# Kernel optimization log

Hardware: AMD Instinct MI355X
Metric: run time of the kernel (lower is better)

The kernel has to match this reference:

```python
import jax, jax.numpy as jnp
import numpy as np

IN_C, OUT_C, K = 32, 3, 4
FT_DIM = IN_C // 2            # 16
LIN_IN = 4 + FT_DIM           # 20
D = IN_C * OUT_C * K * K      # 1536
D8, D4, D2 = D // 8, D // 4, D // 2


def _geometry(h_in, w_in, h_out, w_out, k):
    # numpy replica of get_offset_scale (all-static shapes)
    ih = np.arange(1, h_out + 1, dtype=np.float32)
    iw = np.arange(1, w_out + 1, dtype=np.float32)
    sh, sw = float(h_out) / h_in, float(w_out) / w_in
    ch = ih / sh + 0.5 * (1 - 1 / sh) - 1.0
    cw = iw / sw + 0.5 * (1 - 1 / sw) - 1.0
    s = -((k - 1) // 2)
    gh = np.floor(np.floor(ch)[:, None] + np.arange(s, k + s, dtype=np.float32)).reshape(-1)
    gw = np.floor(np.floor(cw)[:, None] + np.arange(s, k + s, dtype=np.float32)).reshape(-1)
    IH, IW = np.meshgrid(gh, gw, indexing='ij')                 # [h*k, w*k]
    indice = np.stack([IH, IW], -1).reshape(h_out, k, w_out, k, 2).transpose(0, 2, 1, 3, 4)  # [h,w,k,k,2]
    CH, CW = np.meshgrid(ch, cw, indexing='ij')
    center_hw = np.stack([CH, CW], -1).reshape(h_out, w_out, 1, 1, 2)
    c = -s
    offset = indice[:, :, c:c + 1, c:c + 1] - center_hw          # [h,w,1,1,2]
    off_scale = np.concatenate([
        offset,
        np.full((h_out, w_out, 1, 1, 1), sh, np.float32),
        np.full((h_out, w_out, 1, 1, 1), sw, np.float32)], -1).transpose(4, 0, 1, 2, 3)  # [4,h,w,1,1]
    ind = indice.astype(np.int64)
    center_ind = np.floor(center_hw).astype(np.int64)
    pad = int(max(-ind.min(), max((ind[..., 0] - h_in + 1).max(), (ind[..., 1] - w_in + 1).max())))
    return jnp.asarray(off_scale, jnp.float32), ind, center_ind, pad


def _pad_select(t, ind, pad):
    tp = jnp.pad(t, ((0, 0), (0, 0), (pad, pad), (pad, pad)), mode='reflect')
    return tp[:, :, ind[..., 0] + pad, ind[..., 1] + pad]   # [bs,C,*ind.shape[:-1]]


def setup_inputs() -> dict:
    key = jax.random.key(0)
    ks = jax.random.split(key, 16)
    p = lambda k, shp, sc: (jax.random.normal(k, shp, jnp.float32) * sc)
    inp = {
        'lr_features': jax.random.normal(ks[0], (2, IN_C, 48, 48), jnp.float32),
        'kernel_pc': jax.random.normal(ks[1], (2, 10, 48, 48), jnp.float32),
        'h_out': 192, 'w_out': 192,
        'ft_w': p(ks[2], (FT_DIM, IN_C, 4, 4), 0.05), 'ft_b': jnp.zeros((FT_DIM,), jnp.float32),
        'l1w1': p(ks[3], (LIN_IN, D8), 0.1), 'l1b1': jnp.zeros((D8,), jnp.float32),
        'l1w2': p(ks[4], (D8, D8), 0.05), 'l1b2': jnp.zeros((D8,), jnp.float32),
        'l2w1': p(ks[5], (LIN_IN, D8), 0.1), 'l2b1': jnp.zeros((D8,), jnp.float32),
        'l2w2': p(ks[6], (D8, D8), 0.05), 'l2b2': jnp.zeros((D8,), jnp.float32),
        'l3w1': p(ks[7], (D4, D2), 0.03), 'l3b1': jnp.zeros((D2,), jnp.float32),
        'l3w2': p(ks[8], (D2, D), 0.02), 'l3b2': jnp.zeros((D,), jnp.float32),
    }
    return inp


def reference(lr_features, kernel_pc, h_out, w_out, ft_w, ft_b,
              l1w1, l1b1, l1w2, l1b2, l2w1, l2b1, l2w2, l2b2,
              l3w1, l3b1, l3w2, l3b2):
    bs, cn, h_in, w_in = lr_features.shape
    off_scale, ind, center_ind, pad = _geometry(h_in, w_in, h_out, w_out, K)

    # gather kernel_size^2 neighbor pixels per output location
    sel = _pad_select(lr_features, ind, pad)                    # [bs,cn,h,w,K,K]
    sel = sel.transpose(0, 2, 3, 1, 4, 5).reshape(bs, h_out, w_out, cn * K * K)

    # feature_trans conv (reflect pad (1,2,1,2), 4x4, VALID)
    xp = jnp.pad(lr_features, ((0, 0), (0, 0), (1, 2), (1, 2)), mode='reflect')
    ft = jax.lax.conv_general_dilated(xp, ft_w, (1, 1), 'VALID',
                                      dimension_numbers=('NCHW', 'OIHW', 'NCHW'))
    ft = ft + ft_b[None, :, None, None]                         # [bs,FT_DIM,h_in,w_in]

    srf = _pad_select(ft, center_ind, pad)                      # [bs,FT_DIM,h,w,1,1]
    osb = jnp.broadcast_to(off_scale[None], (bs, 4, h_out, w_out, 1, 1))
    osf = jnp.concatenate([srf, osb], axis=1)[..., 0, 0].transpose(0, 2, 3, 1)  # [bs,h,w,LIN_IN]

    # offscale2weight: per-pixel MLP producing dynamic conv weights
    f1 = jnp.tanh(osf @ l1w1 + l1b1) @ l1w2 + l1b2
    f2 = jnp.tanh(osf @ l2w1 + l2b1) @ l2w2 + l2b2
    f = jnp.tanh(jnp.concatenate([f1 * f2, f1], axis=-1))
    f = f @ l3w1 + l3b1
    f = jnp.where(f > 0, f, 0.01 * f)                           # LeakyReLU
    w = (f @ l3w2 + l3b2).reshape(bs, h_out, w_out, OUT_C, cn * K * K)

    out = jnp.einsum('bhwk,bhwok->bhwo', sel, w)                # slice_mul
    return jnp.tanh(out.transpose(0, 3, 1, 2))                  # [bs,OUT_C,h_out,w_out]
```

## Files before the change

kernel.cpp:

```cpp
#include <hip/hip_runtime.h>
#include <math.h>

#define H_IN   48
#define W_IN   48
#define INC    32
#define OUTC   3
#define FT     16
#define Dn     1536
#define D8n    192
#define D4n    384
#define D2n    768

typedef _Float16 h16;
typedef _Float16 f16x8 __attribute__((ext_vector_type(8)));
typedef _Float16 f16x4 __attribute__((ext_vector_type(4)));
typedef float    f32x4 __attribute__((ext_vector_type(4)));

#define MFMA16(a, b, c) __builtin_amdgcn_mfma_f32_16x16x32_f16((a), (b), (c), 0, 0, 0)

__device__ __forceinline__ int reflect48(int i) {
    return (i < 0) ? -i : ((i > 47) ? 94 - i : i);
}

__device__ __forceinline__ float tanhf_fast(float x) {
    float e = __expf(2.f * x);
    return 1.f - 2.f / (e + 1.f);
}

#define SWZ(p, bc) ((bc) ^ (((p) & 7) << 4))

__global__ __launch_bounds__(256) void ft_kernel(const float* __restrict__ lr,
                                                 const float* __restrict__ ft_w,
                                                 const float* __restrict__ ft_b,
                                                 float* __restrict__ ftmap) {
    int idx = blockIdx.x * 256 + threadIdx.x;
    if (idx >= 2 * FT * H_IN * W_IN) return;
    int x = idx % W_IN;
    int y = (idx / W_IN) % H_IN;
    int o = (idx / (W_IN * H_IN)) % FT;
    int bb = idx / (W_IN * H_IN * FT);
    float acc = ft_b[o];
    for (int c = 0; c < INC; ++c) {
        const float* lrc = lr + ((bb * INC + c) * H_IN) * W_IN;
        const float* wc  = ft_w + ((o * INC + c) * 4) * 4;
        #pragma unroll
        for (int dy = 0; dy < 4; ++dy) {
            int ry = reflect48(y + dy - 1);
            #pragma unroll
            for (int dx = 0; dx < 4; ++dx) {
                int rx = reflect48(x + dx - 1);
                acc += lrc[ry * W_IN + rx] * wc[dy * 4 + dx];
            }
        }
    }
    ftmap[idx] = acc;
}

__global__ __launch_bounds__(256) void prep_kernel(const float* __restrict__ l1w2,
                                                   const float* __restrict__ l2w2,
                                                   const float* __restrict__ l3w1,
                                                   const float* __restrict__ l3w2,
                                                   h16* __restrict__ w12t, h16* __restrict__ w22t,
                                                   h16* __restrict__ w31t, h16* __restrict__ w32t) {
    __shared__ float tile[32][33];
    int bid = blockIdx.x;
    const float* src; h16* dst; int K, N, t0;
    if (bid < 36)      { src = l1w2; dst = w12t; K = 192; N = 192;  t0 = 0; }
    else if (bid < 72) { src = l2w2; dst = w22t; K = 192; N = 192;  t0 = 36; }
    else if (bid < 360){ src = l3w1; dst = w31t; K = 384; N = 768;  t0 = 72; }
    else               { src = l3w2; dst = w32t; K = 768; N = 1536; t0 = 360; }
    int t = bid - t0;
    int ntx = N >> 5;
    int kt = t / ntx, nt = t - kt * ntx;
    int k0 = kt << 5, n0 = nt << 5;
    int tx = threadIdx.x & 31, ty = threadIdx.x >> 5;
    #pragma unroll
    for (int i = 0; i < 4; ++i)
        tile[ty + i * 8][tx] = src[(k0 + ty + i * 8) * N + n0 + tx];
    __syncthreads();
    #pragma unroll
    for (int i = 0; i < 4; ++i)
        dst[(n0 + ty + i * 8) * K + k0 + tx] = (h16)tile[tx][ty + i * 8];
}

#define A_OFF_H1   0
#define A_OFF_H2   12288
#define A_OFF_OSF  24576
#define A_OFF_F    0
#define A_OFF_G    0
#define A_S_BYTES  49152

__global__ __launch_bounds__(256, 3) void fused_a(
    const float* __restrict__ ftmap,
    const float* __restrict__ l1w1, const float* __restrict__ l1b1,
    const float* __restrict__ l2w1, const float* __restrict__ l2b1,
    const float* __restrict__ l1b2, const float* __restrict__ l2b2,
    const float* __restrict__ l3b1,
    const h16* __restrict__ W12T, const h16* __restrict__ W22T,
    const h16* __restrict__ W31T,
    h16* __restrict__ Gf)
{
    __shared__ __align__(16) char S[A_S_BYTES];

    const int tid  = threadIdx.x;
    const int lane = tid & 63;
    const int wv   = tid >> 6;
    const int bid  = blockIdx.x;
    const int b    = bid / 1152;
    const int rem  = bid % 1152;
    const int h    = rem / 6;
    const int w0   = (rem % 6) * 32;

    const float ch = (h + 1) * 0.25f - 0.625f;
    const int   fh = (int)floorf(ch);
    const float offh = (float)fh - ch;
    const int   rfh = reflect48(fh);

    float* s_osf = (float*)(S + A_OFF_OSF);

    if (tid < 32) {
        int w = w0 + tid;
        float cw = (w + 1) * 0.25f - 0.625f;
        int fw = (int)floorf(cw);
        float* o = s_osf + tid * 20;
        o[16] = offh; o[17] = (float)fw - cw; o[18] = 4.f; o[19] = 4.f;
    }
    {
        int p = tid >> 3;
        int c0 = (tid & 7) * 2;
        int w = w0 + p;
        float cw = (w + 1) * 0.25f - 0.625f;
        int rfw = reflect48((int)floorf(cw));
        float* o = s_osf + p * 20;
        o[c0]     = ftmap[((b * FT + c0) * H_IN + rfh) * W_IN + rfw];
        o[c0 + 1] = ftmap[((b * FT + c0 + 1) * H_IN + rfh) * W_IN + rfw];
    }
    __syncthreads();

    for (int idx = tid; idx < 2 * 32 * D8n; idx += 256) {
        int br = idx / 6144;
        int r2 = idx - br * 6144;
        int p  = r2 / D8n;
        int j  = r2 - p * D8n;
        const float* W = br ? l2w1 : l1w1;
        const float* B = br ? l2b1 : l1b1;
        const float* o = s_osf + p * 20;
        float acc = B[j];
        #pragma unroll
        for (int i = 0; i < 20; ++i) acc += o[i] * W[i * D8n + j];
        int base = br ? A_OFF_H2 : A_OFF_H1;
        *(h16*)(S + base + p * 384 + SWZ(p, j * 2)) = (h16)tanhf_fast(acc);
    }
    __syncthreads();

    f16x8 Ah[2][2][6];
    {
        int pr = lane & 15, kg = (lane >> 4) << 3;
        #pragma unroll
        for (int br = 0; br < 2; ++br)
            #pragma unroll
            for (int rt = 0; rt < 2; ++rt) {
                int p = rt * 16 + pr;
                #pragma unroll
                for (int kf = 0; kf < 6; ++kf) {
                    int k0 = kf * 32 + kg;
                    Ah[br][rt][kf] = *(const f16x8*)(S + (br ? A_OFF_H2 : A_OFF_H1) + p * 384 + SWZ(p, k0 * 2));
                }
            }
    }
    __syncthreads();

    {
        int pr = lane & 15, kg = (lane >> 4) << 3;
        #pragma unroll
        for (int cc = 0; cc < 3; ++cc) {
            int c = wv * 3 + cc;
            int n = c * 16 + pr;
            f32x4 a00 = {0.f,0.f,0.f,0.f}, a01 = a00, a10 = a00, a11 = a00;
            #pragma unroll
            for (int kf = 0; kf < 6; ++kf) {
                int koff = kf * 32 + kg;
                f16x8 b0 = *(const f16x8*)(W12T + n * D8n + koff);
                f16x8 b1 = *(const f16x8*)(W22T + n * D8n + koff);
                a00 = MFMA16(Ah[0][0][kf], b0, a00);
                a01 = MFMA16(Ah[0][1][kf], b0, a01);
                a10 = MFMA16(Ah[1][0][kf], b1, a10);
                a11 = MFMA16(Ah[1][1][kf], b1, a11);
            }
            float bf1 = l1b2[n], bf2 = l2b2[n];
            #pragma unroll
            for (int rt = 0; rt < 2; ++rt) {
                #pragma unroll
                for (int r = 0; r < 4; ++r) {
                    int p = rt * 16 + ((lane >> 4) << 2) + r;
                    float f1 = (rt ? a01[r] : a00[r]) + bf1;
                    float f2 = (rt ? a11[r] : a10[r]) + bf2;
                    *(h16*)(S + A_OFF_F + p * 768 + SWZ(p, n * 2))         = (h16)tanhf_fast(f1 * f2);
                    *(h16*)(S + A_OFF_F + p * 768 + SWZ(p, (n + D8n) * 2)) = (h16)tanhf_fast(f1);
                }
            }
        }
    }
    __syncthreads();

    f16x8 Af[2][12];
    {
        int pr = lane & 15, kg = (lane >> 4) << 3;
        #pragma unroll
        for (int rt = 0; rt < 2; ++rt) {
            int p = rt * 16 + pr;
            #pragma unroll
            for (int kf = 0; kf < 12; ++kf) {
                int k0 = kf * 32 + kg;
                Af[rt][kf] = *(const f16x8*)(S + A_OFF_F + p * 768 + SWZ(p, k0 * 2));
            }
        }
    }
    __syncthreads();

    {
        int pr = lane & 15, kg = (lane >> 4) << 3;
        #pragma unroll
        for (int q = 0; q < 3; ++q) {
            int ntb = wv * 12 + q * 4;
            f32x4 acc[4][2];
            #pragma unroll
            for (int nn = 0; nn < 4; ++nn) { acc[nn][0] = (f32x4){0.f,0.f,0.f,0.f}; acc[nn][1] = acc[nn][0]; }
            for (int kf = 0; kf < 12; ++kf) {
                int koff = kf * 32 + kg;
                f16x8 bq[4];
                #pragma unroll
                for (int nn = 0; nn < 4; ++nn)
                    bq[nn] = *(const f16x8*)(W31T + ((ntb + nn) * 16 + pr) * D4n + koff);
                #pragma unroll
                for (int nn = 0; nn < 4; ++nn) {
                    acc[nn][0] = MFMA16(Af[0][kf], bq[nn], acc[nn][0]);
                    acc[nn][1] = MFMA16(Af[1][kf], bq[nn], acc[nn][1]);
                }
            }
            #pragma unroll
            for (int nn = 0; nn < 4; ++nn) {
                int n = (ntb + nn) * 16 + pr;
                float bb = l3b1[n];
                #pragma unroll
                for (int rt = 0; rt < 2; ++rt) {
                    #pragma unroll
                    for (int r = 0; r < 4; ++r) {
                        int p = rt * 16 + ((lane >> 4) << 2) + r;
                        float gv = acc[nn][rt][r] + bb;
                        gv = (gv > 0.f) ? gv : 0.01f * gv;
                        *(h16*)(S + A_OFF_G + p * 1536 + SWZ(p, n * 2)) = (h16)gv;
                    }
                }
            }
        }
    }
    __syncthreads();

    {
        int pr = lane & 15, kg = lane >> 4;
        int ptg0 = (b * 192 + h) * 12 + (w0 >> 4);
        #pragma unroll
        for (int i = 0; i < 12; ++i) {
            int pair = wv * 12 + i;
            int rt = pair / 24, kf = pair % 24;
            int p = rt * 16 + pr;
            f16x8 v = *(const f16x8*)(S + A_OFF_G + p * 1536 + SWZ(p, (kf * 32 + kg * 8) * 2));
            size_t e = ((size_t)((ptg0 + rt) * 24 + kf) * 4 + kg) * 16 + pr;
            *(f16x8*)(Gf + e * 8) = v;
        }
    }
}

#define B_S_BYTES (65536 + 6144)

__global__ __launch_bounds__(512, 4) void gemm_b(
    const float* __restrict__ lr,
    const h16* __restrict__ Gf,
    const h16* __restrict__ W32T,
    const float* __restrict__ l3b2,
    float* __restrict__ out)
{
    __shared__ __align__(16) char S[B_S_BYTES];
    float* s_red = (float*)(S + 65536);

    const int tid  = threadIdx.x;
    const int lane = tid & 63;
    const int wvv  = tid >> 6;
    const int pr   = lane & 15;
    const int kg   = lane >> 4;

    const int bid = blockIdx.x;
    const int b   = bid / 576;
    const int rem = bid % 576;
    const int h   = rem / 3;
    const int w0  = (rem % 3) * 64;

    const float chh = (h + 1) * 0.25f - 0.625f;
    const int fh = (int)floorf(chh);

    {
        int k = tid;
        int c = k >> 4, k1 = (k >> 2) & 3, k2 = k & 3;
        int rh = reflect48(fh - 1 + k1);
        const float* lrrow = lr + ((b * INC + c) * H_IN + rh) * W_IN;
        #pragma unroll 8
        for (int p = 0; p < 64; ++p) {
            float cw = (w0 + p + 1) * 0.25f - 0.625f;
            int fw = (int)floorf(cw);
            float v = lrrow[reflect48(fw - 1 + k2)];
            *(h16*)(S + p * 1024 + ((k * 2) ^ ((p & 7) << 4))) = (h16)v;
        }
    }
    __syncthreads();

    const int ptB = (b * 192 + h) * 12 + (w0 >> 4);
    const int nt0 = wvv * 12;

    float acc0[4], acc1[4], acc2[4];
    #pragma unroll
    for (int pt = 0; pt < 4; ++pt) { acc0[pt] = 0.f; acc1[pt] = 0.f; acc2[pt] = 0.f; }

    const h16* Gbase = Gf + ((size_t)(kg * 16 + pr)) * 8;

    for (int cc2 = 0; cc2 < 12; ++cc2) {
        f16x8 gB[4][2];
        #pragma unroll
        for (int pt = 0; pt < 4; ++pt)
            #pragma unroll
            for (int kf = 0; kf < 2; ++kf)
                gB[pt][kf] = *(const f16x8*)(Gbase + ((size_t)((ptB + pt) * 24 + (cc2 * 2 + kf)) * 64) * 8);

        for (int i = 0; i < 12; ++i) {
            int nt = nt0 + i;
            int oc = nt >> 5;
            int kbase = (nt & 31) * 16 + kg * 4;

            const h16* wrow = W32T + (size_t)(nt * 16 + pr) * D2n + cc2 * 64 + kg * 8;
            f16x8 Wa0 = *(const f16x8*)(wrow);
            f16x8 Wa1 = *(const f16x8*)(wrow + 32);

            f32x4 wacc[4];
            #pragma unroll
            for (int pt = 0; pt < 4; ++pt) {
                wacc[pt] = (f32x4){0.f,0.f,0.f,0.f};
                wacc[pt] = MFMA16(Wa0, gB[pt][0], wacc[pt]);
                wacc[pt] = MFMA16(Wa1, gB[pt][1], wacc[pt]);
            }

            float4 b2v;
            if (cc2 == 0) b2v = *(const float4*)(l3b2 + nt * 16 + kg * 4);

            if (oc == 0) {
                #pragma unroll
                for (int pt = 0; pt < 4; ++pt) {
                    int p = pt * 16 + pr;
                    f16x4 sl = *(const f16x4*)(S + p * 1024 + ((kbase * 2) ^ ((p & 7) << 4)));
                    #pragma unroll
                    for (int r = 0; r < 4; ++r) {
                        float sv = (float)sl[r];
                        acc0[pt] += wacc[pt][r] * sv;
                        if (cc2 == 0) acc0[pt] += ((const float*)&b2v)[r] * sv;
                    }
                }
            } else if (oc == 1) {
                #pragma unroll
                for (int pt = 0; pt < 4; ++pt) {
                    int p = pt * 16 + pr;
                    f16x4 sl = *(const f16x4*)(S + p * 1024 + ((kbase * 2) ^ ((p & 7) << 4)));
                    #pragma unroll
                    for (int r = 0; r < 4; ++r) {
                        float sv = (float)sl[r];
                        acc1[pt] += wacc[pt][r] * sv;
                        if (cc2 == 0) acc1[pt] += ((const float*)&b2v)[r] * sv;
                    }
                }
            } else {
                #pragma unroll
                for (int pt = 0; pt < 4; ++pt) {
                    int p = pt * 16 + pr;
                    f16x4 sl = *(const f16x4*)(S + p * 1024 + ((kbase * 2) ^ ((p & 7) << 4)));
                    #pragma unroll
                    for (int r = 0; r < 4; ++r) {
                        float sv = (float)sl[r];
                        acc2[pt] += wacc[pt][r] * sv;
                        if (cc2 == 0) acc2[pt] += ((const float*)&b2v)[r] * sv;
                    }
                }
            }
        }
    }

    #pragma unroll
    for (int pt = 0; pt < 4; ++pt) {
        float v0 = acc0[pt], v1 = acc1[pt], v2 = acc2[pt];
        v0 += __shfl_xor(v0, 16); v0 += __shfl_xor(v0, 32);
        v1 += __shfl_xor(v1, 16); v1 += __shfl_xor(v1, 32);
        v2 += __shfl_xor(v2, 16); v2 += __shfl_xor(v2, 32);
        if (lane < 16) {
            float* r = s_red + ((size_t)wvv * 64 + pt * 16 + pr) * 3;
            r[0] = v0; r[1] = v1; r[2] = v2;
        }
    }
    __syncthreads();
    if (tid < 192) {
        int p = tid / 3, oc = tid % 3;
        float s = 0.f;
        #pragma unroll
        for (int wv2 = 0; wv2 < 8; ++wv2) s += s_red[((size_t)wv2 * 64 + p) * 3 + oc];
        out[((b * OUTC + oc) * 192 + h) * 192 + (w0 + p)] = tanhf_fast(s);
    }
}

__global__ __launch_bounds__(256, 2) void fused_fallback(
    const float* __restrict__ lr, const float* __restrict__ ftmap,
    const float* __restrict__ l1w1, const float* __restrict__ l1b1,
    const float* __restrict__ l2w1, const float* __restrict__ l2b1,
    const float* __restrict__ l1b2, const float* __restrict__ l2b2,
    const float* __restrict__ l3b1, const float* __restrict__ l3b2,
    const h16* __restrict__ W12T, const h16* __restrict__ W22T,
    const h16* __restrict__ W31T, const h16* __restrict__ W32T,
    float* __restrict__ out)
{
    __shared__ __align__(16) char S[63104];
    const int tid  = threadIdx.x;
    const int lane = tid & 63;
    const int wv   = tid >> 6;
    const int bid  = blockIdx.x;
    const int b    = bid / 1152;
    const int rem  = bid % 1152;
    const int h    = rem / 6;
    const int w0   = (rem % 6) * 32;

    const float ch = (h + 1) * 0.25f - 0.625f;
    const int   fh = (int)floorf(ch);
    const float offh = (float)fh - ch;
    const int   rfh = reflect48(fh);

    float* s_osf = (float*)(S + 24576);
    unsigned char* s_sc = (unsigned char*)(S + 61440);
    h16*   s_lrr = (h16*)(S + 49152);
    float* s_red = (float*)(S + 61568);

    if (tid < 128) {
        int p = tid >> 2, k2 = tid & 3;
        int w = w0 + p;
        float cw = (w + 1) * 0.25f - 0.625f;
        int fw = (int)floorf(cw);
        s_sc[p * 4 + k2] = (unsigned char)reflect48(fw - 1 + k2);
        if (k2 == 0) {
            float* o = s_osf + p * 20;
            o[16] = offh; o[17] = (float)fw - cw; o[18] = 4.f; o[19] = 4.f;
        }
    }
    {
        int p = tid >> 3;
        int c0 = (tid & 7) * 2;
        int w = w0 + p;
        float cw = (w + 1) * 0.25f - 0.625f;
        int rfw = reflect48((int)floorf(cw));
        float* o = s_osf + p * 20;
        o[c0]     = ftmap[((b * FT + c0) * H_IN + rfh) * W_IN + rfw];
        o[c0 + 1] = ftmap[((b * FT + c0 + 1) * H_IN + rfh) * W_IN + rfw];
    }
    for (int idx = tid; idx < 32 * 4 * 48; idx += 256) {
        int c = idx / 192, r2 = idx - c * 192, k1 = r2 / 48, col = r2 - k1 * 48;
        int row = reflect48(fh - 1 + k1);
        s_lrr[idx] = (h16)lr[((b * INC + c) * H_IN + row) * W_IN + col];
    }
    for (int idx = tid; idx < 4 * 32 * 3; idx += 256) s_red[idx] = 0.f;
    __syncthreads();

    for (int idx = tid; idx < 2 * 32 * D8n; idx += 256) {
        int br = idx / 6144;
        int r2 = idx - br * 6144;
        int p  = r2 / D8n;
        int j  = r2 - p * D8n;
        const float* W = br ? l2w1 : l1w1;
        const float* B = br ? l2b1 : l1b1;
        const float* o = s_osf + p * 20;
        float acc = B[j];
        #pragma unroll
        for (int i = 0; i < 20; ++i) acc += o[i] * W[i * D8n + j];
        int base = br ? 12288 : 0;
        *(h16*)(S + base + p * 384 + SWZ(p, j * 2)) = (h16)tanhf_fast(acc);
    }
    __syncthreads();

    f16x8 Ah[2][2][6];
    {
        int pr = lane & 15, kg = (lane >> 4) << 3;
        #pragma unroll
        for (int br = 0; br < 2; ++br)
            #pragma unroll
            for (int rt = 0; rt < 2; ++rt) {
                int p = rt * 16 + pr;
                #pragma unroll
                for (int kf = 0; kf < 6; ++kf)
                    Ah[br][rt][kf] = *(const f16x8*)(S + (br ? 12288 : 0) + p * 384 + SWZ(p, (kf * 32 + kg) * 2));
            }
    }
    __syncthreads();

    {
        int pr = lane & 15, kg = (lane >> 4) << 3;
        #pragma unroll
        for (int cc = 0; cc < 3; ++cc) {
            int c = wv * 3 + cc;
            int n = c * 16 + pr;
            f32x4 a00 = {0.f,0.f,0.f,0.f}, a01 = a00, a10 = a00, a11 = a00;
            #pragma unroll
            for (int kf = 0; kf < 6; ++kf) {
                int koff = kf * 32 + kg;
                f16x8 b0 = *(const f16x8*)(W12T + n * D8n + koff);
                f16x8 b1 = *(const f16x8*)(W22T + n * D8n + koff);
                a00 = MFMA16(Ah[0][0][kf], b0, a00);
                a01 = MFMA16(Ah[0][1][kf], b0, a01);
                a10 = MFMA16(Ah[1][0][kf], b1, a10);
                a11 = MFMA16(Ah[1][1][kf], b1, a11);
            }
            float bf1 = l1b2[n], bf2 = l2b2[n];
            #pragma unroll
            for (int rt = 0; rt < 2; ++rt)
                #pragma unroll
                for (int r = 0; r < 4; ++r) {
                    int p = rt * 16 + ((lane >> 4) << 2) + r;
                    float f1 = (rt ? a01[r] : a00[r]) + bf1;
                    float f2 = (rt ? a11[r] : a10[r]) + bf2;
                    *(h16*)(S + p * 768 + SWZ(p, n * 2))         = (h16)tanhf_fast(f1 * f2);
                    *(h16*)(S + p * 768 + SWZ(p, (n + D8n) * 2)) = (h16)tanhf_fast(f1);
                }
        }
    }
    __syncthreads();

    f16x8 Af[2][12];
    {
        int pr = lane & 15, kg = (lane >> 4) << 3;
        #pragma unroll
        for (int rt = 0; rt < 2; ++rt) {
            int p = rt * 16 + pr;
            #pragma unroll
            for (int kf = 0; kf < 12; ++kf)
                Af[rt][kf] = *(const f16x8*)(S + p * 768 + SWZ(p, (kf * 32 + kg) * 2));
        }
    }
    __syncthreads();

    {
        int pr = lane & 15, kg = (lane >> 4) << 3;
        #pragma unroll
        for (int q = 0; q < 3; ++q) {
            int ntb = wv * 12 + q * 4;
            f32x4 acc[4][2];
            #pragma unroll
            for (int nn = 0; nn < 4; ++nn) { acc[nn][0] = (f32x4){0.f,0.f,0.f,0.f}; acc[nn][1] = acc[nn][0]; }
            for (int kf = 0; kf < 12; ++kf) {
                int koff = kf * 32 + kg;
                f16x8 bq[4];
                #pragma unroll
                for (int nn = 0; nn < 4; ++nn)
                    bq[nn] = *(const f16x8*)(W31T + ((ntb + nn) * 16 + pr) * D4n + koff);
                #pragma unroll
                for (int nn = 0; nn < 4; ++nn) {
                    acc[nn][0] = MFMA16(Af[0][kf], bq[nn], acc[nn][0]);
                    acc[nn][1] = MFMA16(Af[1][kf], bq[nn], acc[nn][1]);
                }
            }
            #pragma unroll
            for (int nn = 0; nn < 4; ++nn) {
                int n = (ntb + nn) * 16 + pr;
                float bb = l3b1[n];
                #pragma unroll
                for (int rt = 0; rt < 2; ++rt)
                    #pragma unroll
                    for (int r = 0; r < 4; ++r) {
                        int p = rt * 16 + ((lane >> 4) << 2) + r;
                        float gv = acc[nn][rt][r] + bb;
                        gv = (gv > 0.f) ? gv : 0.01f * gv;
                        *(h16*)(S + p * 1536 + SWZ(p, n * 2)) = (h16)gv;
                    }
            }
        }
    }
    __syncthreads();

    {
        int pr = lane & 15, kg = (lane >> 4) << 3;
        float acc8[2][4];
        #pragma unroll
        for (int rt = 0; rt < 2; ++rt)
            #pragma unroll
            for (int r = 0; r < 4; ++r) acc8[rt][r] = 0.f;
        int cur_oc = (wv * 24) >> 5;

        for (int q = 0; q < 6; ++q) {
            int ntb = wv * 24 + q * 4;
            int oc = ntb >> 5;
            if (oc != cur_oc) {
                #pragma unroll
                for (int rt = 0; rt < 2; ++rt)
                    #pragma unroll
                    for (int r = 0; r < 4; ++r) {
                        float v = acc8[rt][r];
                        v += __shfl_xor(v, 1); v += __shfl_xor(v, 2);
                        v += __shfl_xor(v, 4); v += __shfl_xor(v, 8);
                        if ((lane & 15) == 0) {
                            int p = rt * 16 + ((lane >> 4) << 2) + r;
                            s_red[(wv * 32 + p) * 3 + cur_oc] += v;
                        }
                        acc8[rt][r] = 0.f;
                    }
                cur_oc = oc;
            }
            f32x4 acc[4][2];
            #pragma unroll
            for (int nn = 0; nn < 4; ++nn) { acc[nn][0] = (f32x4){0.f,0.f,0.f,0.f}; acc[nn][1] = acc[nn][0]; }
            for (int kf = 0; kf < 24; ++kf) {
                int koff = kf * 32 + kg;
                f16x8 a0 = *(const f16x8*)(S + pr * 1536 + SWZ(pr, koff * 2));
                int p1 = 16 + pr;
                f16x8 a1 = *(const f16x8*)(S + p1 * 1536 + SWZ(p1, koff * 2));
                f16x8 bq[4];
                #pragma unroll
                for (int nn = 0; nn < 4; ++nn)
                    bq[nn] = *(const f16x8*)(W32T + ((ntb + nn) * 16 + pr) * D2n + koff);
                #pragma unroll
                for (int nn = 0; nn < 4; ++nn) {
                    acc[nn][0] = MFMA16(a0, bq[nn], acc[nn][0]);
                    acc[nn][1] = MFMA16(a1, bq[nn], acc[nn][1]);
                }
            }
            #pragma unroll
            for (int nn = 0; nn < 4; ++nn) {
                int n = (ntb + nn) * 16 + pr;
                float wb = l3b2[n];
                int k  = n & 511;
                int c  = k >> 4, k1 = (k >> 2) & 3, k2 = k & 3;
                const h16* lrr = s_lrr + (c * 4 + k1) * 48;
                #pragma unroll
                for (int rt = 0; rt < 2; ++rt)
                    #pragma unroll
                    for (int r = 0; r < 4; ++r) {
                        int p = rt * 16 + ((lane >> 4) << 2) + r;
                        float sv = (float)lrr[s_sc[p * 4 + k2]];
                        acc8[rt][r] += (acc[nn][rt][r] + wb) * sv;
                    }
            }
        }
        #pragma unroll
        for (int rt = 0; rt < 2; ++rt)
            #pragma unroll
            for (int r = 0; r < 4; ++r) {
                float v = acc8[rt][r];
                v += __shfl_xor(v, 1); v += __shfl_xor(v, 2);
                v += __shfl_xor(v, 4); v += __shfl_xor(v, 8);
                if ((lane & 15) == 0) {
                    int p = rt * 16 + ((lane >> 4) << 2) + r;
                    s_red[(wv * 32 + p) * 3 + cur_oc] += v;
                }
            }
    }
    __syncthreads();

    if (tid < 96) {
        int p = tid / 3, oc = tid % 3;
        float s = s_red[(0 * 32 + p) * 3 + oc] + s_red[(1 * 32 + p) * 3 + oc]
                + s_red[(2 * 32 + p) * 3 + oc] + s_red[(3 * 32 + p) * 3 + oc];
        out[((b * OUTC + oc) * 192 + h) * 192 + (w0 + p)] = tanhf_fast(s);
    }
}

extern "C" void kernel_launch(void* const* d_in, const int* in_sizes, int n_in,
                              void* d_out, int out_size, void* d_ws, size_t ws_size,
                              hipStream_t stream) {
    const float* lr   = (const float*)d_in[0];
    const float* ft_w = (const float*)d_in[4];
    const float* ft_b = (const float*)d_in[5];
    const float* l1w1 = (const float*)d_in[6];
    const float* l1b1 = (const float*)d_in[7];
    const float* l1w2 = (const float*)d_in[8];
    const float* l1b2 = (const float*)d_in[9];
    const float* l2w1 = (const float*)d_in[10];
    const float* l2b1 = (const float*)d_in[11];
    const float* l2w2 = (const float*)d_in[12];
    const float* l2b2 = (const float*)d_in[13];
    const float* l3w1 = (const float*)d_in[14];
    const float* l3b1 = (const float*)d_in[15];
    const float* l3w2 = (const float*)d_in[16];
    const float* l3b2 = (const float*)d_in[17];
    float* outp = (float*)d_out;

    char* ws = (char*)d_ws;
    float* ftmap = (float*)(ws + 0);
    h16* w12t = (h16*)(ws + 294912);
    h16* w22t = (h16*)(ws + 368640);
    h16* w31t = (h16*)(ws + 442368);
    h16* w32t = (h16*)(ws + 1032192);
    h16* Gf   = (h16*)(ws + 3391488);

    hipLaunchKernelGGL(prep_kernel, dim3(1512), dim3(256), 0, stream,
                       l1w2, l2w2, l3w1, l3w2, w12t, w22t, w31t, w32t);
    hipLaunchKernelGGL(ft_kernel, dim3(288), dim3(256), 0, stream, lr, ft_w, ft_b, ftmap);

    if (ws_size >= (size_t)116637696) {
        hipLaunchKernelGGL(fused_a, dim3(2304), dim3(256), 0, stream,
                           ftmap, l1w1, l1b1, l2w1, l2b1,
                           l1b2, l2b2, l3b1,
                           w12t, w22t, w31t, Gf);
        hipLaunchKernelGGL(gemm_b, dim3(1152), dim3(512), 0, stream,
                           lr, Gf, w32t, l3b2, outp);
    } else {
        hipLaunchKernelGGL(fused_fallback, dim3(2304), dim3(256), 0, stream,
                           lr, ftmap,
                           l1w1, l1b1, l2w1, l2b1,
                           l1b2, l2b2, l3b1, l3b2,
                           w12t, w22t, w31t, w32t,
                           outp);
    }
}
```

Before: 692.8 us.

## Accumulate MFMA weight tiles across full K before applying slice multiply

```diff
diff --git a/kernel.cpp b/kernel.cpp
--- a/kernel.cpp
+++ b/kernel.cpp
@@ -323,33 +323,41 @@
 
     const h16* Gbase = Gf + ((size_t)(kg * 16 + pr)) * 8;
 
-    for (int cc2 = 0; cc2 < 12; ++cc2) {
-        f16x8 gB[4][2];
-        #pragma unroll
-        for (int pt = 0; pt < 4; ++pt)
-            #pragma unroll
-            for (int kf = 0; kf < 2; ++kf)
-                gB[pt][kf] = *(const f16x8*)(Gbase + ((size_t)((ptB + pt) * 24 + (cc2 * 2 + kf)) * 64) * 8);
-
-        for (int i = 0; i < 12; ++i) {
-            int nt = nt0 + i;
+    for (int grp = 0; grp < 6; ++grp) {
+        f32x4 wacc[2][4];
+        #pragma unroll
+        for (int i = 0; i < 2; ++i)
+            #pragma unroll
+            for (int pt = 0; pt < 4; ++pt) wacc[i][pt] = (f32x4){0.f,0.f,0.f,0.f};
+
+        for (int cc2 = 0; cc2 < 12; ++cc2) {
+            f16x8 gB[4][2];
+            #pragma unroll
+            for (int pt = 0; pt < 4; ++pt)
+                #pragma unroll
+                for (int kf = 0; kf < 2; ++kf)
+                    gB[pt][kf] = *(const f16x8*)(Gbase + ((size_t)((ptB + pt) * 24 + (cc2 * 2 + kf)) * 64) * 8);
+
+            #pragma unroll
+            for (int i = 0; i < 2; ++i) {
+                int nt = nt0 + grp * 2 + i;
+                const h16* wrow = W32T + (size_t)(nt * 16 + pr) * D2n + cc2 * 64 + kg * 8;
+                f16x8 Wa0 = *(const f16x8*)(wrow);
+                f16x8 Wa1 = *(const f16x8*)(wrow + 32);
+                #pragma unroll
+                for (int pt = 0; pt < 4; ++pt) {
+                    wacc[i][pt] = MFMA16(Wa0, gB[pt][0], wacc[i][pt]);
+                    wacc[i][pt] = MFMA16(Wa1, gB[pt][1], wacc[i][pt]);
+                }
+            }
+        }
+
+        #pragma unroll
+        for (int i = 0; i < 2; ++i) {
+            int nt = nt0 + grp * 2 + i;
             int oc = nt >> 5;
             int kbase = (nt & 31) * 16 + kg * 4;
-
-            const h16* wrow = W32T + (size_t)(nt * 16 + pr) * D2n + cc2 * 64 + kg * 8;
-            f16x8 Wa0 = *(const f16x8*)(wrow);
-            f16x8 Wa1 = *(const f16x8*)(wrow + 32);
-
-            f32x4 wacc[4];
-            #pragma unroll
-            for (int pt = 0; pt < 4; ++pt) {
-                wacc[pt] = (f32x4){0.f,0.f,0.f,0.f};
-                wacc[pt] = MFMA16(Wa0, gB[pt][0], wacc[pt]);
-                wacc[pt] = MFMA16(Wa1, gB[pt][1], wacc[pt]);
-            }
-
-            float4 b2v;
-            if (cc2 == 0) b2v = *(const float4*)(l3b2 + nt * 16 + kg * 4);
+            float4 b2v = *(const float4*)(l3b2 + nt * 16 + kg * 4);
 
             if (oc == 0) {
                 #pragma unroll
@@ -357,11 +365,8 @@
                     int p = pt * 16 + pr;
                     f16x4 sl = *(const f16x4*)(S + p * 1024 + ((kbase * 2) ^ ((p & 7) << 4)));
                     #pragma unroll
-                    for (int r = 0; r < 4; ++r) {
-                        float sv = (float)sl[r];
-                        acc0[pt] += wacc[pt][r] * sv;
-                        if (cc2 == 0) acc0[pt] += ((const float*)&b2v)[r] * sv;
-                    }
+                    for (int r = 0; r < 4; ++r)
+                        acc0[pt] += (wacc[i][pt][r] + ((const float*)&b2v)[r]) * (float)sl[r];
                 }
             } else if (oc == 1) {
                 #pragma unroll
@@ -369,11 +374,8 @@
                     int p = pt * 16 + pr;
                     f16x4 sl = *(const f16x4*)(S + p * 1024 + ((kbase * 2) ^ ((p & 7) << 4)));
                     #pragma unroll
-                    for (int r = 0; r < 4; ++r) {
-                        float sv = (float)sl[r];
-                        acc1[pt] += wacc[pt][r] * sv;
-                        if (cc2 == 0) acc1[pt] += ((const float*)&b2v)[r] * sv;
-                    }
+                    for (int r = 0; r < 4; ++r)
+                        acc1[pt] += (wacc[i][pt][r] + ((const float*)&b2v)[r]) * (float)sl[r];
                 }
             } else {
                 #pragma unroll
@@ -381,11 +383,8 @@
                     int p = pt * 16 + pr;
                     f16x4 sl = *(const f16x4*)(S + p * 1024 + ((kbase * 2) ^ ((p & 7) << 4)));
                     #pragma unroll
-                    for (int r = 0; r < 4; ++r) {
-                        float sv = (float)sl[r];
-                        acc2[pt] += wacc[pt][r] * sv;
-                        if (cc2 == 0) acc2[pt] += ((const float*)&b2v)[r] * sv;
-                    }
+                    for (int r = 0; r < 4; ++r)
+                        acc2[pt] += (wacc[i][pt][r] + ((const float*)&b2v)[r]) * (float)sl[r];
                 }
             }
         }
```

Result: slower. 1.709 ms (+146.7%).

## Restructure final GEMM loop: two K-chunks per pass, two pixel tiles per sweep

Applied to the files above, without the earlier changes.

```diff
diff --git a/kernel.cpp b/kernel.cpp
--- a/kernel.cpp
+++ b/kernel.cpp
@@ -323,73 +323,61 @@
 
     const h16* Gbase = Gf + ((size_t)(kg * 16 + pr)) * 8;
 
-    for (int cc2 = 0; cc2 < 12; ++cc2) {
-        f16x8 gB[4][2];
-        #pragma unroll
-        for (int pt = 0; pt < 4; ++pt)
-            #pragma unroll
-            for (int kf = 0; kf < 2; ++kf)
-                gB[pt][kf] = *(const f16x8*)(Gbase + ((size_t)((ptB + pt) * 24 + (cc2 * 2 + kf)) * 64) * 8);
-
-        for (int i = 0; i < 12; ++i) {
-            int nt = nt0 + i;
-            int oc = nt >> 5;
-            int kbase = (nt & 31) * 16 + kg * 4;
-
-            const h16* wrow = W32T + (size_t)(nt * 16 + pr) * D2n + cc2 * 64 + kg * 8;
-            f16x8 Wa0 = *(const f16x8*)(wrow);
-            f16x8 Wa1 = *(const f16x8*)(wrow + 32);
-
-            f32x4 wacc[4];
-            #pragma unroll
-            for (int pt = 0; pt < 4; ++pt) {
-                wacc[pt] = (f32x4){0.f,0.f,0.f,0.f};
-                wacc[pt] = MFMA16(Wa0, gB[pt][0], wacc[pt]);
-                wacc[pt] = MFMA16(Wa1, gB[pt][1], wacc[pt]);
-            }
-
-            float4 b2v;
-            if (cc2 == 0) b2v = *(const float4*)(l3b2 + nt * 16 + kg * 4);
-
-            if (oc == 0) {
-                #pragma unroll
-                for (int pt = 0; pt < 4; ++pt) {
-                    int p = pt * 16 + pr;
-                    f16x4 sl = *(const f16x4*)(S + p * 1024 + ((kbase * 2) ^ ((p & 7) << 4)));
+    #define EPI(ACC)                                                              \
+        _Pragma("unroll")                                                         \
+        for (int ptl = 0; ptl < 2; ++ptl) {                                       \
+            const int pt = ptp * 2 + ptl;                                         \
+            const int p  = pt * 16 + pr;                                          \
+            f16x4 sl = *(const f16x4*)(S + p * 1024 + ((kbase * 2) ^ ((p & 7) << 4))); \
+            _Pragma("unroll")                                                     \
+            for (int r = 0; r < 4; ++r)                                           \
+                ACC[pt] += wacc[ptl][r] * (float)sl[r];                           \
+            if (grp == 0) {                                                       \
+                float4 b2v = *(const float4*)(l3b2 + nt * 16 + kg * 4);           \
+                _Pragma("unroll")                                                 \
+                for (int r = 0; r < 4; ++r)                                       \
+                    ACC[pt] += ((const float*)&b2v)[r] * (float)sl[r];            \
+            }                                                                     \
+        }
+
+    #pragma unroll
+    for (int ptp = 0; ptp < 2; ++ptp) {
+        for (int grp = 0; grp < 6; ++grp) {
+            f16x8 gB[2][2][2];
+            #pragma unroll
+            for (int ptl = 0; ptl < 2; ++ptl)
+                #pragma unroll
+                for (int cl = 0; cl < 2; ++cl)
                     #pragma unroll
-                    for (int r = 0; r < 4; ++r) {
-                        float sv = (float)sl[r];
-                        acc0[pt] += wacc[pt][r] * sv;
-                        if (cc2 == 0) acc0[pt] += ((const float*)&b2v)[r] * sv;
+                    for (int kf = 0; kf < 2; ++kf)
+                        gB[ptl][cl][kf] = *(const f16x8*)(Gbase +
+                            ((size_t)((ptB + ptp * 2 + ptl) * 24 + ((grp * 2 + cl) * 2 + kf)) * 64) * 8);
+
+            for (int i = 0; i < 12; ++i) {
+                int nt = nt0 + i;
+                f32x4 wacc[2];
+                wacc[0] = (f32x4){0.f,0.f,0.f,0.f};
+                wacc[1] = (f32x4){0.f,0.f,0.f,0.f};
+                #pragma unroll
+                for (int cl = 0; cl < 2; ++cl) {
+                    const h16* wrow = W32T + (size_t)(nt * 16 + pr) * D2n + (grp * 2 + cl) * 64 + kg * 8;
+                    f16x8 Wa0 = *(const f16x8*)(wrow);
+                    f16x8 Wa1 = *(const f16x8*)(wrow + 32);
+                    #pragma unroll
+                    for (int ptl = 0; ptl < 2; ++ptl) {
+                        wacc[ptl] = MFMA16(Wa0, gB[ptl][cl][0], wacc[ptl]);
+                        wacc[ptl] = MFMA16(Wa1, gB[ptl][cl][1], wacc[ptl]);
                     }
                 }
-            } else if (oc == 1) {
-                #pragma unroll
-                for (int pt = 0; pt < 4; ++pt) {
-                    int p = pt * 16 + pr;
-                    f16x4 sl = *(const f16x4*)(S + p * 1024 + ((kbase * 2) ^ ((p & 7) << 4)));
-                    #pragma unroll
-                    for (int r = 0; r < 4; ++r) {
-                        float sv = (float)sl[r];
-                        acc1[pt] += wacc[pt][r] * sv;
-                        if (cc2 == 0) acc1[pt] += ((const float*)&b2v)[r] * sv;
-                    }
-                }
-            } else {
-                #pragma unroll
-                for (int pt = 0; pt < 4; ++pt) {
-                    int p = pt * 16 + pr;
-                    f16x4 sl = *(const f16x4*)(S + p * 1024 + ((kbase * 2) ^ ((p & 7) << 4)));
-                    #pragma unroll
-                    for (int r = 0; r < 4; ++r) {
-                        float sv = (float)sl[r];
-                        acc2[pt] += wacc[pt][r] * sv;
-                        if (cc2 == 0) acc2[pt] += ((const float*)&b2v)[r] * sv;
-                    }
-                }
-            }
-        }
-    }
+                int oc    = nt >> 5;
+                int kbase = (nt & 31) * 16 + kg * 4;
+                if (oc == 0)      { EPI(acc0) }
+                else if (oc == 1) { EPI(acc1) }
+                else              { EPI(acc2) }
+            }
+        }
+    }
+    #undef EPI
 
     #pragma unroll
     for (int pt = 0; pt < 4; ++pt) {
```

After: 1.031 ms. +48.8%, slower.

## Split K across waves instead of N tiles, keep G fragments in registers

Applied to the files above, without the earlier changes.

```diff
diff --git a/kernel.cpp b/kernel.cpp
--- a/kernel.cpp
+++ b/kernel.cpp
@@ -314,82 +314,114 @@
     }
     __syncthreads();
 
+    {
+        int p = tid >> 3, part = tid & 7;
+        const char* selrow = (const char*)S + p * 1024;
+        float s0 = 0.f, s1 = 0.f, s2 = 0.f;
+        #pragma unroll
+        for (int j = 0; j < 16; ++j) {
+            int k = part * 64 + j * 4;
+            f16x4 sl = *(const f16x4*)(selrow + ((k * 2) ^ ((p & 7) << 4)));
+            float4 ba = *(const float4*)(l3b2 + k);
+            float4 bbv = *(const float4*)(l3b2 + 512 + k);
+            float4 bc = *(const float4*)(l3b2 + 1024 + k);
+            #pragma unroll
+            for (int r = 0; r < 4; ++r) {
+                float sv = (float)sl[r];
+                s0 += ((const float*)&ba)[r]  * sv;
+                s1 += ((const float*)&bbv)[r] * sv;
+                s2 += ((const float*)&bc)[r]  * sv;
+            }
+        }
+        float* rr = s_red + ((size_t)part * 64 + p) * 3;
+        rr[0] = s0; rr[1] = s1; rr[2] = s2;
+    }
+    __syncthreads();
+
     const int ptB = (b * 192 + h) * 12 + (w0 >> 4);
-    const int nt0 = wvv * 12;
+
+    f16x8 gB[4][3];
+    {
+        const h16* Gbase = Gf + (size_t)(kg * 16 + pr) * 8;
+        #pragma unroll
+        for (int pt = 0; pt < 4; ++pt)
+            #pragma unroll
+            for (int kfl = 0; kfl < 3; ++kfl)
+                gB[pt][kfl] = *(const f16x8*)(Gbase +
+                    ((size_t)((ptB + pt) * 24 + (wvv * 3 + kfl)) * 64) * 8);
+    }
+
+    const h16* Wbase = W32T + (size_t)pr * D2n + wvv * 96 + kg * 8;
 
     float acc0[4], acc1[4], acc2[4];
     #pragma unroll
     for (int pt = 0; pt < 4; ++pt) { acc0[pt] = 0.f; acc1[pt] = 0.f; acc2[pt] = 0.f; }
 
-    const h16* Gbase = Gf + ((size_t)(kg * 16 + pr)) * 8;
-
-    for (int cc2 = 0; cc2 < 12; ++cc2) {
-        f16x8 gB[4][2];
-        #pragma unroll
-        for (int pt = 0; pt < 4; ++pt)
-            #pragma unroll
-            for (int kf = 0; kf < 2; ++kf)
-                gB[pt][kf] = *(const f16x8*)(Gbase + ((size_t)((ptB + pt) * 24 + (cc2 * 2 + kf)) * 64) * 8);
-
-        for (int i = 0; i < 12; ++i) {
-            int nt = nt0 + i;
-            int oc = nt >> 5;
-            int kbase = (nt & 31) * 16 + kg * 4;
-
-            const h16* wrow = W32T + (size_t)(nt * 16 + pr) * D2n + cc2 * 64 + kg * 8;
-            f16x8 Wa0 = *(const f16x8*)(wrow);
-            f16x8 Wa1 = *(const f16x8*)(wrow + 32);
-
-            f32x4 wacc[4];
-            #pragma unroll
-            for (int pt = 0; pt < 4; ++pt) {
-                wacc[pt] = (f32x4){0.f,0.f,0.f,0.f};
-                wacc[pt] = MFMA16(Wa0, gB[pt][0], wacc[pt]);
-                wacc[pt] = MFMA16(Wa1, gB[pt][1], wacc[pt]);
-            }
-
-            float4 b2v;
-            if (cc2 == 0) b2v = *(const float4*)(l3b2 + nt * 16 + kg * 4);
-
-            if (oc == 0) {
-                #pragma unroll
-                for (int pt = 0; pt < 4; ++pt) {
-                    int p = pt * 16 + pr;
-                    f16x4 sl = *(const f16x4*)(S + p * 1024 + ((kbase * 2) ^ ((p & 7) << 4)));
-                    #pragma unroll
-                    for (int r = 0; r < 4; ++r) {
-                        float sv = (float)sl[r];
-                        acc0[pt] += wacc[pt][r] * sv;
-                        if (cc2 == 0) acc0[pt] += ((const float*)&b2v)[r] * sv;
-                    }
-                }
-            } else if (oc == 1) {
-                #pragma unroll
-                for (int pt = 0; pt < 4; ++pt) {
-                    int p = pt * 16 + pr;
-                    f16x4 sl = *(const f16x4*)(S + p * 1024 + ((kbase * 2) ^ ((p & 7) << 4)));
-                    #pragma unroll
-                    for (int r = 0; r < 4; ++r) {
-                        float sv = (float)sl[r];
-                        acc1[pt] += wacc[pt][r] * sv;
-                        if (cc2 == 0) acc1[pt] += ((const float*)&b2v)[r] * sv;
-                    }
-                }
-            } else {
-                #pragma unroll
-                for (int pt = 0; pt < 4; ++pt) {
-                    int p = pt * 16 + pr;
-                    f16x4 sl = *(const f16x4*)(S + p * 1024 + ((kbase * 2) ^ ((p & 7) << 4)));
-                    #pragma unroll
-                    for (int r = 0; r < 4; ++r) {
-                        float sv = (float)sl[r];
-                        acc2[pt] += wacc[pt][r] * sv;
-                        if (cc2 == 0) acc2[pt] += ((const float*)&b2v)[r] * sv;
-                    }
-                }
-            }
-        }
-    }
+    const f32x4 z4 = {0.f, 0.f, 0.f, 0.f};
+
+    f16x8 WaA0, WaA1, WaA2, WaB0, WaB1, WaB2;
+    WaA0 = *(const f16x8*)(Wbase);
+    WaA1 = *(const f16x8*)(Wbase + 32);
+    WaA2 = *(const f16x8*)(Wbase + 64);
+
+    #define STEP(NT, W0_, W1_, W2_, N0_, N1_, N2_, ACC) {                          \
+        int ntn_ = (NT) + 1; ntn_ = (ntn_ > 95) ? 95 : ntn_;                       \
+        const h16* wp_ = Wbase + (size_t)ntn_ * (16 * D2n);                        \
+        N0_ = *(const f16x8*)(wp_);                                                \
+        N1_ = *(const f16x8*)(wp_ + 32);                                           \
+        N2_ = *(const f16x8*)(wp_ + 64);                                           \
+        f32x4 w0_ = MFMA16(W0_, gB[0][0], z4);                                     \
+        f32x4 w1_ = MFMA16(W0_, gB[1][0], z4);                                     \
+        f32x4 w2_ = MFMA16(W0_, gB[2][0], z4);                                     \
+        f32x4 w3_ = MFMA16(W0_, gB[3][0], z4);                                     \
+        w0_ = MFMA16(W1_, gB[0][1], w0_);                                          \
+        w1_ = MFMA16(W1_, gB[1][1], w1_);                                          \
+        w2_ = MFMA16(W1_, gB[2][1], w2_);                                          \
+        w3_ = MFMA16(W1_, gB[3][1], w3_);                                          \
+        w0_ = MFMA16(W2_, gB[0][2], w0_);                                          \
+        w1_ = MFMA16(W2_, gB[1][2], w1_);                                          \
+        w2_ = MFMA16(W2_, gB[2][2], w2_);                                          \
+        w3_ = MFMA16(W2_, gB[3][2], w3_);                                          \
+        const int kbase_ = ((NT) & 31) * 16 + kg * 4;                              \
+        {                                                                          \
+            const int p_ = pr;                                                     \
+            f16x4 sl_ = *(const f16x4*)(S + p_ * 1024 + ((kbase_ * 2) ^ ((p_ & 7) << 4))); \
+            ACC[0] += w0_[0]*(float)sl_[0] + w0_[1]*(float)sl_[1]                  \
+                    + w0_[2]*(float)sl_[2] + w0_[3]*(float)sl_[3];                 \
+        }                                                                          \
+        {                                                                          \
+            const int p_ = 16 + pr;                                                \
+            f16x4 sl_ = *(const f16x4*)(S + p_ * 1024 + ((kbase_ * 2) ^ ((p_ & 7) << 4))); \
+            ACC[1] += w1_[0]*(float)sl_[0] + w1_[1]*(float)sl_[1]                  \
+                    + w1_[2]*(float)sl_[2] + w1_[3]*(float)sl_[3];                 \
+        }                                                                          \
+        {                                                                          \
+            const int p_ = 32 + pr;                                                \
+            f16x4 sl_ = *(const f16x4*)(S + p_ * 1024 + ((kbase_ * 2) ^ ((p_ & 7) << 4))); \
+            ACC[2] += w2_[0]*(float)sl_[0] + w2_[1]*(float)sl_[1]                  \
+                    + w2_[2]*(float)sl_[2] + w2_[3]*(float)sl_[3];                 \
+        }                                                                          \
+        {                                                                          \
+            const int p_ = 48 + pr;                                                \
+            f16x4 sl_ = *(const f16x4*)(S + p_ * 1024 + ((kbase_ * 2) ^ ((p_ & 7) << 4))); \
+            ACC[3] += w3_[0]*(float)sl_[0] + w3_[1]*(float)sl_[1]                  \
+                    + w3_[2]*(float)sl_[2] + w3_[3]*(float)sl_[3];                 \
+        }                                                                          \
+    }
+
+    for (int t = 0; t < 16; ++t) {
+        STEP(2*t,     WaA0, WaA1, WaA2, WaB0, WaB1, WaB2, acc0)
+        STEP(2*t + 1, WaB0, WaB1, WaB2, WaA0, WaA1, WaA2, acc0)
+    }
+    for (int t = 16; t < 32; ++t) {
+        STEP(2*t,     WaA0, WaA1, WaA2, WaB0, WaB1, WaB2, acc1)
+        STEP(2*t + 1, WaB0, WaB1, WaB2, WaA0, WaA1, WaA2, acc1)
+    }
+    for (int t = 32; t < 48; ++t) {
+        STEP(2*t,     WaA0, WaA1, WaA2, WaB0, WaB1, WaB2, acc2)
+        STEP(2*t + 1, WaB0, WaB1, WaB2, WaA0, WaA1, WaA2, acc2)
+    }
+    #undef STEP
 
     #pragma unroll
     for (int pt = 0; pt < 4; ++pt) {
@@ -399,7 +431,7 @@
         v2 += __shfl_xor(v2, 16); v2 += __shfl_xor(v2, 32);
         if (lane < 16) {
             float* r = s_red + ((size_t)wvv * 64 + pt * 16 + pr) * 3;
-            r[0] = v0; r[1] = v1; r[2] = v2;
+            r[0] += v0; r[1] += v1; r[2] += v2;
         }
     }
     __syncthreads();
```

New measurement: 698.7 us. Within noise of the previous version (+0.8%).
